# Performance work log

Measured on AMD Instinct MI355X. Metric: run time of the kernel, lower is better.

The kernel has to match this reference:

```python
import jax, jax.numpy as jnp
import numpy as np

BS, NPOINT, N, C = 2, 128, 8192, 128
NUM_CLASS, HEAD_BINS, K = 3, 12, 64
MLP1, MLP2, IOU_H = 128, 256, 128
EPS_BN = 1e-5


def setup_inputs():
    key = jax.random.key(0)
    ks = jax.random.split(key, 16)
    rn = lambda k, s, sc=1.0: jax.random.normal(k, s, jnp.float32) * sc
    return {
        'original_xyz': rn(ks[0], (BS, N, 3), 10.0),
        'original_feature': rn(ks[1], (BS, C, N)),
        'candidate_xyz': rn(ks[2], (BS, NPOINT, 3), 10.0),
        'pred_cls': rn(ks[3], (BS, NPOINT, NUM_CLASS)),
        'pred_offsets': rn(ks[4], (BS, NPOINT, 6)),
        'pred_angle_cls': rn(ks[5], (BS, NPOINT, HEAD_BINS)),
        'pred_angle_res': rn(ks[6], (BS, NPOINT, HEAD_BINS), 0.1),
        'w_mlp1': rn(ks[7], (MLP1, C + 3), 0.05), 'b_mlp1': jnp.zeros((MLP1,), jnp.float32),
        'w_mlp2': rn(ks[8], (MLP2, MLP1), 0.05), 'b_mlp2': jnp.zeros((MLP2,), jnp.float32),
        'w_iou0': rn(ks[9], (IOU_H, MLP2), 0.05), 'b_iou0': jnp.zeros((IOU_H,), jnp.float32),
        'g_iou0': jnp.ones((IOU_H,), jnp.float32), 'be_iou0': jnp.zeros((IOU_H,), jnp.float32),
        'w_iou1': rn(ks[10], (IOU_H, IOU_H), 0.05), 'b_iou1': jnp.zeros((IOU_H,), jnp.float32),
        'g_iou1': jnp.ones((IOU_H,), jnp.float32), 'be_iou1': jnp.zeros((IOU_H,), jnp.float32),
        'w_iou2': rn(ks[11], (1, IOU_H), 0.05), 'b_iou2': jnp.zeros((1,), jnp.float32),
    }


def _bn1d(x, g, b):
    # training-mode BatchNorm1d over (batch, length)
    m = jnp.mean(x, (0, 2), keepdims=True)
    v = jnp.var(x, (0, 2), keepdims=True)
    return (x - m) / jnp.sqrt(v + EPS_BN) * g[None, :, None] + b[None, :, None]


def _forward(original_xyz, original_feature, candidate_xyz, pred_cls, pred_offsets,
             pred_angle_cls, pred_angle_res, w_mlp1, b_mlp1, w_mlp2, b_mlp2,
             w_iou0, b_iou0, g_iou0, be_iou0, w_iou1, b_iou1, g_iou1, be_iou1,
             w_iou2, b_iou2):
    sg = jax.lax.stop_gradient
    original_xyz = sg(original_xyz)
    original_feature = sg(original_feature)
    bs, npoint = candidate_xyz.shape[0], candidate_xyz.shape[1]
    # --- decode_prediction (detached in original) ---
    acls = jnp.argmax(pred_angle_cls, -1)                              # [bs,np]
    ares = jnp.take_along_axis(pred_angle_res, acls[..., None], -1)[..., 0]
    apc = 2.0 * np.pi / HEAD_BINS
    angle = acls.astype(jnp.float32) * apc + ares
    heading = sg(jnp.where(angle > np.pi, angle - 2.0 * np.pi, angle))
    center = sg(candidate_xyz + pred_offsets[:, :, :3])
    lwh = sg(jnp.maximum(pred_offsets[:, :, 3:6] * 2.0, 0.1))
    # --- 4x4x4 grid scaled by box dims ---
    gs = jnp.linspace(-1.0, 1.0, 4)
    gx, gy, gz = jnp.meshgrid(gs, gs, gs, indexing='ij')
    grid = jnp.stack([gx.ravel(), gy.ravel(), gz.ravel()], -1)          # [64,3]
    whole_grid = grid[None, None] * lwh[:, :, None, :]                  # [bs,np,64,3]
    # --- rotation about z ---
    c, s = jnp.cos(heading), jnp.sin(heading)
    z = jnp.zeros_like(c); o = jnp.ones_like(c)
    R = jnp.stack([jnp.stack([c, s, z], -1),
                   jnp.stack([-s, c, z], -1),
                   jnp.stack([z, z, o], -1)], -2)                        # [bs,np,3,3]
    rel = jnp.einsum('bpkc,bpcd->bpkd', whole_grid, R)                   # [bs,np,64,3]
    corners = (rel + center[:, :, None, :]).reshape(bs, npoint * K, 3)   # [bs,M,3]
    # --- three_nn: 3 nearest original points per corner ---
    d2 = (jnp.sum(corners ** 2, -1)[:, :, None]
          + jnp.sum(original_xyz ** 2, -1)[:, None, :]
          - 2.0 * jnp.einsum('bmc,bnc->bmn', corners, original_xyz))     # [bs,M,N]
    _, idx = jax.lax.top_k(-d2, 3)                                       # [bs,M,3]
    nn_xyz = jax.vmap(lambda pts, i: pts[i])(original_xyz, idx)          # [bs,M,3,3]
    dist = jnp.sqrt(jnp.sum((nn_xyz - corners[:, :, None, :]) ** 2, -1)) # [bs,M,3]
    w = 1.0 / (dist + 1e-8)
    w = w / jnp.sum(w, -1, keepdims=True)
    nn_feat = jax.vmap(lambda f, i: f[:, i])(original_feature, idx)      # [bs,C,M,3]
    interp = jnp.sum(nn_feat * w[:, None], -1).reshape(bs, -1, npoint, K)
    feat = jnp.concatenate([rel.transpose(0, 3, 1, 2), interp], 1)       # [bs,C+3,np,K]
    # --- CGE shared MLP (1x1 conv + relu) ---
    h = jax.nn.relu(jnp.einsum('oc,bcpk->bopk', w_mlp1, feat) + b_mlp1[None, :, None, None])
    h = jax.nn.relu(jnp.einsum('oc,bcpk->bopk', w_mlp2, h) + b_mlp2[None, :, None, None])
    h = jnp.max(h, -1)                                                   # [bs,256,np]
    # --- IoU head ---
    h = jax.nn.relu(_bn1d(jnp.einsum('oc,bcp->bop', w_iou0, h) + b_iou0[None, :, None], g_iou0, be_iou0))
    h = jax.nn.relu(_bn1d(jnp.einsum('oc,bcp->bop', w_iou1, h) + b_iou1[None, :, None], g_iou1, be_iou1))
    return jnp.einsum('oc,bcp->bop', w_iou2, h) + b_iou2[None, :, None]  # [bs,1,np]


def reference(original_xyz, original_feature, candidate_xyz, pred_cls, pred_offsets,
              pred_angle_cls, pred_angle_res, w_mlp1, b_mlp1, w_mlp2, b_mlp2,
              w_iou0, b_iou0, g_iou0, be_iou0, w_iou1, b_iou1, g_iou1, be_iou1,
              w_iou2, b_iou2):
    return _forward(original_xyz, original_feature, candidate_xyz, pred_cls, pred_offsets,
                    pred_angle_cls, pred_angle_res, w_mlp1, b_mlp1, w_mlp2, b_mlp2,
                    w_iou0, b_iou0, g_iou0, be_iou0, w_iou1, b_iou1, g_iou1, be_iou1,
                    w_iou2, b_iou2)
```

## Files before the change

kernel.cpp:

```cpp
#include <hip/hip_runtime.h>
#include <math.h>

#define BSZ 2
#define NPOINT 128
#define NPTS 8192
#define CH_F 128
#define HEAD_BINS 12
#define KCOR 64
#define MTOT (NPOINT*KCOR)
#define FEAT_C 131
#define MLP2_C 256

#define OFF_CORNERS 0u
#define OFF_REL     196608u
#define OFF_IDX3    393216u
#define OFF_W3      589824u
#define OFF_FEATT   6684672u
#define OFF_W1T     15073280u
#define OFF_W2T     15140352u
#define OFF_XYZP    15271424u
#define OFF_H2      15533568u
#define OFF_X0      15795712u
#define OFF_X1      15926784u
#define OFF_BN0     16057856u
#define OFF_BN1     16058880u

__global__ __launch_bounds__(256) void k_prep(const float* __restrict__ cand, const float* __restrict__ offs,
                        const float* __restrict__ angc, const float* __restrict__ angr,
                        const float* __restrict__ w1, const float* __restrict__ w2,
                        const float* __restrict__ of, const float* __restrict__ xyz,
                        float* __restrict__ corners, float* __restrict__ rel,
                        float* __restrict__ w1t, float* __restrict__ w2t,
                        float* __restrict__ ft, float4* __restrict__ xyzp)
{
    __shared__ float tile[128][17];
    __shared__ float sr[4*KCOR*3];
    __shared__ float sc_[4*KCOR*3];
    int bid = blockIdx.x;
    int t = threadIdx.x;
    if (bid < 64) {
        int b = bid >> 5, p0 = (bid & 31) * 4;
        int lb = t >> 6, k = t & 63;
        int bp = b*NPOINT + p0 + lb;
        const float* ac = angc + bp*HEAD_BINS;
        int best = 0; float bv = ac[0];
        #pragma unroll
        for (int j = 1; j < HEAD_BINS; ++j) { float v = ac[j]; if (v > bv) { bv = v; best = j; } }
        float ares = angr[bp*HEAD_BINS + best];
        float angle = (float)best * 0.52359877559829882f + ares;
        float heading = (angle > 3.14159265358979323f) ? (angle - 6.28318530717958647f) : angle;
        float cx = cand[bp*3+0] + offs[bp*6+0];
        float cy = cand[bp*3+1] + offs[bp*6+1];
        float cz = cand[bp*3+2] + offs[bp*6+2];
        float dl = fmaxf(offs[bp*6+3]*2.0f, 0.1f);
        float dw = fmaxf(offs[bp*6+4]*2.0f, 0.1f);
        float dh = fmaxf(offs[bp*6+5]*2.0f, 0.1f);
        float chd = cosf(heading), shd = sinf(heading);
        int ix = (k>>4)&3, iy = (k>>2)&3, iz = k&3;
        float gx = (ix==3) ? 1.0f : (-1.0f + (2.0f/3.0f)*(float)ix);
        float gy = (iy==3) ? 1.0f : (-1.0f + (2.0f/3.0f)*(float)iy);
        float gz = (iz==3) ? 1.0f : (-1.0f + (2.0f/3.0f)*(float)iz);
        float wx = gx*dl, wy = gy*dw, wz = gz*dh;
        float rx = wx*chd - wy*shd;
        float ry = wx*shd + wy*chd;
        int si = (lb*KCOR + k)*3;
        sr[si+0] = rx;      sr[si+1] = ry;      sr[si+2] = wz;
        sc_[si+0] = rx+cx;  sc_[si+1] = ry+cy;  sc_[si+2] = wz+cz;
        __syncthreads();
        size_t base = ((size_t)b*MTOT + (size_t)p0*KCOR)*3;
        if (t < 192) {
            ((float4*)(rel + base))[t]     = ((const float4*)sr)[t];
            ((float4*)(corners + base))[t] = ((const float4*)sc_)[t];
        }
    } else if (bid < 80) {
        int i0 = (bid-64)*256 + t;
        for (int i = i0; i < FEAT_C*128; i += 16*256) { int o = i & 127, c = i >> 7; w1t[i] = w1[o*FEAT_C + c]; }
        for (int i = i0; i < 128*256;    i += 16*256) { int o = i & 255, c = i >> 8; w2t[i] = w2[o*128 + c]; }
    } else if (bid < 144) {
        int i = (bid-80)*256 + t;
        const float* s = xyz + (size_t)i*3;
        float x = s[0], y = s[1], z = s[2];
        xyzp[i] = make_float4(x, y, z, (x*x + y*y) + z*z);
    } else {
        int bi = bid - 144;
        int b = bi >> 9;
        int n0 = (bi & 511) * 16;
        #pragma unroll
        for (int it = 0; it < 2; ++it) {
            int id = it*256 + t;
            int c = id >> 2, q = id & 3;
            float4 v = *(const float4*)(of + ((size_t)(b*CH_F + c))*NPTS + n0 + q*4);
            tile[c][q*4+0] = v.x; tile[c][q*4+1] = v.y; tile[c][q*4+2] = v.z; tile[c][q*4+3] = v.w;
        }
        __syncthreads();
        #pragma unroll
        for (int it = 0; it < 2; ++it) {
            int id = it*256 + t;
            int n = id >> 5, cq = id & 31;
            float4 o;
            o.x = tile[cq*4+0][n]; o.y = tile[cq*4+1][n]; o.z = tile[cq*4+2][n]; o.w = tile[cq*4+3][n];
            *(float4*)(ft + ((size_t)b*NPTS + n0 + n)*CH_F + cq*4) = o;
        }
    }
}

__global__ __launch_bounds__(512) void k_three_nn(const float4* __restrict__ xyzp,
        const float* __restrict__ cand, const float* __restrict__ offs,
        const float* __restrict__ corners,
        int* __restrict__ idx3, float* __restrict__ w3)
{
    __shared__ unsigned short lidx[NPTS];
    __shared__ float4 ptile[512];
    __shared__ int    itile[512];
    __shared__ float  red[1752];
    __shared__ float  pms[512*3];
    __shared__ int    pmi[512*3];
    __shared__ int    s_cnt;
    __shared__ float  s_T;

    int bid = blockIdx.x;
    int b    = bid >> 8;
    int p    = (bid >> 1) & 127;
    int half = bid & 1;
    int t = threadIdx.x;
    int bp = b*NPOINT + p;

    float cx = cand[bp*3+0] + offs[bp*6+0];
    float cy = cand[bp*3+1] + offs[bp*6+1];
    float cz = cand[bp*3+2] + offs[bp*6+2];
    float dl = fmaxf(offs[bp*6+3]*2.0f, 0.1f);
    float dw = fmaxf(offs[bp*6+4]*2.0f, 0.1f);
    float dh = fmaxf(offs[bp*6+5]*2.0f, 0.1f);
    float H  = sqrtf((dl*dl + dw*dw) + dh*dh);
    float scc = (cx*cx + cy*cy) + cz*cz;

    const float4* xb = xyzp + (size_t)b*NPTS;

    float d2c[16];
    float a0 = 3.4e38f, a1 = 3.4e38f, a2 = 3.4e38f;
    #pragma unroll
    for (int i = 0; i < 16; ++i) {
        float4 P = xb[i*512 + t];
        float dot = fmaf(cz, P.z, fmaf(cy, P.y, cx*P.x));
        float d2 = (scc + P.w) - 2.0f*dot;
        d2c[i] = d2;
        a2 = __builtin_amdgcn_fmed3f(d2, a1, a2);
        a1 = __builtin_amdgcn_fmed3f(d2, a0, a1);
        a0 = fminf(d2, a0);
    }
    red[t*3+0] = a0; red[t*3+1] = a1; red[t*3+2] = a2;
    if (t == 0) s_cnt = 0;
    __syncthreads();
    if (t < 64) {
        float m0 = 3.4e38f, m1 = 3.4e38f, m2 = 3.4e38f;
        for (int s = t*8; s < t*8+8; ++s) {
            #pragma unroll
            for (int j = 0; j < 3; ++j) {
                float v = red[s*3+j];
                m2 = __builtin_amdgcn_fmed3f(v, m1, m2);
                m1 = __builtin_amdgcn_fmed3f(v, m0, m1);
                m0 = fminf(v, m0);
            }
        }
        red[1536 + t*3+0] = m0; red[1536 + t*3+1] = m1; red[1536 + t*3+2] = m2;
    }
    __syncthreads();
    if (t == 0) {
        float m0 = 3.4e38f, m1 = 3.4e38f, m2 = 3.4e38f;
        for (int s = 0; s < 64; ++s) {
            #pragma unroll
            for (int j = 0; j < 3; ++j) {
                float v = red[1536 + s*3+j];
                m2 = __builtin_amdgcn_fmed3f(v, m1, m2);
                m1 = __builtin_amdgcn_fmed3f(v, m0, m1);
                m0 = fminf(v, m0);
            }
        }
        float r3 = sqrtf(fmaxf(m2, 0.0f));
        float rad = r3 + 2.0f*H;
        s_T = rad*rad*1.0002f + 0.25f;
    }
    __syncthreads();

    float T = s_T;
    #pragma unroll
    for (int i = 0; i < 16; ++i) {
        if (d2c[i] <= T) {
            int pos = atomicAdd(&s_cnt, 1);
            lidx[pos] = (unsigned short)(i*512 + t);
        }
    }
    __syncthreads();
    int C = s_cnt;

    int ck  = half*32 + (t >> 4);
    int sub = t & 15;
    size_t crow = (size_t)b*MTOT + p*KCOR + ck;
    float ox = corners[crow*3+0], oy = corners[crow*3+1], oz = corners[crow*3+2];
    float so = (ox*ox + oy*oy) + oz*oz;
    float s0 = 3.4e38f, s1 = 3.4e38f, s2 = 3.4e38f;
    int i0 = 0x7fffffff, i1 = 0x7fffffff, i2 = 0x7fffffff;

    int ntile = (C + 511) >> 9;
    for (int tb = 0; tb < ntile; ++tb) {
        __syncthreads();
        int j = (tb << 9) + t;
        if (j < C) {
            int idx = lidx[j];
            ptile[t] = xb[idx];
            itile[t] = idx;
        } else {
            ptile[t] = make_float4(0.0f, 0.0f, 0.0f, 3.0e38f);
            itile[t] = 0x7fffffff;
        }
        __syncthreads();
        #pragma unroll 4
        for (int k = sub; k < 512; k += 16) {
            float4 P = ptile[k];
            int idx = itile[k];
            float dot = fmaf(oz, P.z, fmaf(oy, P.y, ox*P.x));
            float d2 = (so + P.w) - 2.0f*dot;
            bool lt0 = (d2 < s0) || (d2 == s0 && idx < i0);
            bool lt1 = (d2 < s1) || (d2 == s1 && idx < i1);
            bool lt2 = (d2 < s2) || (d2 == s2 && idx < i2);
            s2 = lt1 ? s1 : (lt2 ? d2  : s2); i2 = lt1 ? i1 : (lt2 ? idx : i2);
            s1 = lt0 ? s0 : (lt1 ? d2  : s1); i1 = lt0 ? i0 : (lt1 ? idx : i1);
            s0 = lt0 ? d2 : s0;               i0 = lt0 ? idx : i0;
        }
    }
    pms[t*3+0] = s0; pms[t*3+1] = s1; pms[t*3+2] = s2;
    pmi[t*3+0] = i0; pmi[t*3+1] = i1; pmi[t*3+2] = i2;
    __syncthreads();

    if (t < 32) {
        float f0 = 3.4e38f, f1 = 3.4e38f, f2 = 3.4e38f;
        int   j0 = 0x7fffffff, j1 = 0x7fffffff, j2 = 0x7fffffff;
        for (int tt = t*16; tt < t*16+16; ++tt) {
            #pragma unroll
            for (int j = 0; j < 3; ++j) {
                float d = pms[tt*3+j]; int id = pmi[tt*3+j];
                bool lt0 = (d < f0) || (d == f0 && id < j0);
                bool lt1 = (d < f1) || (d == f1 && id < j1);
                bool lt2 = (d < f2) || (d == f2 && id < j2);
                f2 = lt1 ? f1 : (lt2 ? d  : f2); j2 = lt1 ? j1 : (lt2 ? id : j2);
                f1 = lt0 ? f0 : (lt1 ? d  : f1); j1 = lt0 ? j0 : (lt1 ? id : j1);
                f0 = lt0 ? d  : f0;              j0 = lt0 ? id : j0;
            }
        }
        int ckf = half*32 + t;
        size_t row = (size_t)b*MTOT + p*KCOR + ckf;
        float qx = corners[row*3+0], qy = corners[row*3+1], qz = corners[row*3+2];
        int ii[3] = {j0, j1, j2};
        float w[3];
        #pragma unroll
        for (int j = 0; j < 3; ++j) {
            float4 P = xb[ii[j]];
            float dx = P.x - qx, dy = P.y - qy, dz = P.z - qz;
            float dist = sqrtf((dx*dx + dy*dy) + dz*dz);
            w[j] = 1.0f/(dist + 1e-8f);
        }
        float wsum = (w[0]+w[1])+w[2];
        #pragma unroll
        for (int j = 0; j < 3; ++j) {
            idx3[row*3+j] = ii[j];
            w3[row*3+j]   = w[j]/wsum;
        }
    }
}

__global__ __launch_bounds__(512) void k_mlp(const int* __restrict__ idx3, const float* __restrict__ w3,
        const float* __restrict__ featT, const float* __restrict__ rel,
        const float* __restrict__ w1t, const float* __restrict__ b1,
        const float* __restrict__ w2t, const float* __restrict__ b2,
        float* __restrict__ h2)
{
    __shared__ float lds[FEAT_C*64];
    __shared__ float swt[3][64];
    __shared__ int   sidx[3][64];
    int blk = blockIdx.x; int b = blk >> 7, p = blk & 127;
    int t = threadIdx.x;
    int g0 = b*MTOT + p*KCOR;

    if (t < 64) {
        size_t row = (size_t)(g0 + t)*3;
        #pragma unroll
        for (int j = 0; j < 3; ++j) { sidx[j][t] = idx3[row+j]; swt[j][t] = w3[row+j]; }
    } else if (t < 256) {
        int u = t - 64;
        lds[(u % 3)*64 + (u / 3)] = rel[(size_t)g0*3 + u];
    }
    __syncthreads();

    const float4* fb = (const float4*)(featT + (size_t)b*NPTS*CH_F);
    #pragma unroll
    for (int it = 0; it < 4; ++it) {
        int idx = it*512 + t;
        int cq = idx >> 6, m = idx & 63;
        int j0 = sidx[0][m], j1 = sidx[1][m], j2 = sidx[2][m];
        float w0 = swt[0][m], w1 = swt[1][m], w2 = swt[2][m];
        float4 f0 = fb[(size_t)j0*32 + cq];
        float4 f1 = fb[(size_t)j1*32 + cq];
        float4 f2 = fb[(size_t)j2*32 + cq];
        float4 v;
        v.x = (f0.x*w0 + f1.x*w1) + f2.x*w2;
        v.y = (f0.y*w0 + f1.y*w1) + f2.y*w2;
        v.z = (f0.z*w0 + f1.z*w1) + f2.z*w2;
        v.w = (f0.w*w0 + f1.w*w1) + f2.w*w2;
        int c0 = 3 + cq*4;
        lds[(c0+0)*64+m] = v.x; lds[(c0+1)*64+m] = v.y;
        lds[(c0+2)*64+m] = v.z; lds[(c0+3)*64+m] = v.w;
    }
    __syncthreads();

    int og = t >> 4, mg = t & 15;
    float acc[4][4];
    #pragma unroll
    for (int i = 0; i < 4; ++i) { float bb = b1[og*4+i];
        #pragma unroll
        for (int j = 0; j < 4; ++j) acc[i][j] = bb; }
    #pragma unroll 4
    for (int c = 0; c < FEAT_C; ++c) {
        float4 wv = *(const float4*)(w1t + c*128 + og*4);
        float4 f0 = *(const float4*)(&lds[c*64 + mg*4]);
        float fv[4] = {f0.x,f0.y,f0.z,f0.w};
        float wa[4] = {wv.x,wv.y,wv.z,wv.w};
        #pragma unroll
        for (int i = 0; i < 4; ++i)
            #pragma unroll
            for (int j = 0; j < 4; ++j)
                acc[i][j] = fmaf(wa[i], fv[j], acc[i][j]);
    }
    __syncthreads();
    #pragma unroll
    for (int i = 0; i < 4; ++i) {
        float4 r0 = make_float4(fmaxf(acc[i][0],0.f), fmaxf(acc[i][1],0.f), fmaxf(acc[i][2],0.f), fmaxf(acc[i][3],0.f));
        *(float4*)(&lds[(og*4+i)*64 + mg*4]) = r0;
    }
    __syncthreads();

    int og2 = t >> 3, mg2 = t & 7;
    float a2[4][8];
    #pragma unroll
    for (int i = 0; i < 4; ++i) { float bb = b2[og2*4+i];
        #pragma unroll
        for (int j = 0; j < 8; ++j) a2[i][j] = bb; }
    #pragma unroll 2
    for (int c = 0; c < 128; ++c) {
        float4 wv = *(const float4*)(w2t + c*MLP2_C + og2*4);
        float4 f0 = *(const float4*)(&lds[c*64 + mg2*8]);
        float4 f1 = *(const float4*)(&lds[c*64 + mg2*8 + 4]);
        float fv[8] = {f0.x,f0.y,f0.z,f0.w,f1.x,f1.y,f1.z,f1.w};
        float wa[4] = {wv.x,wv.y,wv.z,wv.w};
        #pragma unroll
        for (int i = 0; i < 4; ++i)
            #pragma unroll
            for (int j = 0; j < 8; ++j)
                a2[i][j] = fmaf(wa[i], fv[j], a2[i][j]);
    }
    float mx[4];
    #pragma unroll
    for (int i = 0; i < 4; ++i) {
        float m0 = a2[i][0];
        #pragma unroll
        for (int j = 1; j < 8; ++j) m0 = fmaxf(m0, a2[i][j]);
        mx[i] = fmaxf(m0, 0.0f);
    }
    #pragma unroll
    for (int off = 1; off < 8; off <<= 1)
        #pragma unroll
        for (int i = 0; i < 4; ++i)
            mx[i] = fmaxf(mx[i], __shfl_xor(mx[i], off, 64));
    if (mg2 == 0)
        *(float4*)(&h2[((size_t)b*NPOINT + p)*MLP2_C + og2*4]) = make_float4(mx[0],mx[1],mx[2],mx[3]);
}

__global__ __launch_bounds__(256) void k_head0(const float* __restrict__ h2, const float* __restrict__ w0,
                        const float* __restrict__ b0, const float* __restrict__ g0,
                        const float* __restrict__ be0,
                        float* __restrict__ x0, float* __restrict__ bn0)
{
    __shared__ float ssum[256], ssq[256];
    int o = blockIdx.x;
    int t = threadIdx.x;
    int b = t >> 7, p = t & 127;
    const float4* hb = (const float4*)(h2 + ((size_t)b*NPOINT + p)*MLP2_C);
    const float4* wr = (const float4*)(w0 + (size_t)o*MLP2_C);
    float acc = b0[o];
    #pragma unroll 8
    for (int cq = 0; cq < 64; ++cq) {
        float4 h = hb[cq], w = wr[cq];
        acc = fmaf(h.x, w.x, acc); acc = fmaf(h.y, w.y, acc);
        acc = fmaf(h.z, w.z, acc); acc = fmaf(h.w, w.w, acc);
    }
    x0[((size_t)b*NPOINT + p)*128 + o] = acc;
    ssum[t] = acc; ssq[t] = acc*acc;
    __syncthreads();
    if (t < 128) { ssum[t] += ssum[t+128]; ssq[t] += ssq[t+128]; }
    __syncthreads();
    if (t < 64) {
        float s = ssum[t] + ssum[t+64];
        float q = ssq[t] + ssq[t+64];
        #pragma unroll
        for (int off = 32; off >= 1; off >>= 1) {
            s += __shfl_down(s, off, 64);
            q += __shfl_down(q, off, 64);
        }
        if (t == 0) {
            float mean = s * (1.0f/256.0f);
            float var  = q * (1.0f/256.0f) - mean*mean;
            if (var < 0.f) var = 0.f;
            float scale = g0[o] / sqrtf(var + 1e-5f);
            bn0[o]       = scale;
            bn0[128 + o] = be0[o] - mean*scale;
        }
    }
}

__global__ __launch_bounds__(256) void k_head1(const float* __restrict__ x0, const float* __restrict__ bn0,
                        const float* __restrict__ w1, const float* __restrict__ b1,
                        const float* __restrict__ g1, const float* __restrict__ be1,
                        float* __restrict__ x1, float* __restrict__ bn1)
{
    __shared__ float ssum[256], ssq[256];
    int o = blockIdx.x;
    int t = threadIdx.x;
    int b = t >> 7, p = t & 127;
    const float4* xb = (const float4*)(x0 + ((size_t)b*NPOINT + p)*128);
    const float4* wr = (const float4*)(w1 + (size_t)o*128);
    float acc = b1[o];
    #pragma unroll 8
    for (int cq = 0; cq < 32; ++cq) {
        float4 xv = xb[cq], wv = wr[cq];
        float4 sc = *(const float4*)(bn0 + cq*4);
        float4 sh = *(const float4*)(bn0 + 128 + cq*4);
        acc = fmaf(wv.x, fmaxf(fmaf(xv.x, sc.x, sh.x), 0.0f), acc);
        acc = fmaf(wv.y, fmaxf(fmaf(xv.y, sc.y, sh.y), 0.0f), acc);
        acc = fmaf(wv.z, fmaxf(fmaf(xv.z, sc.z, sh.z), 0.0f), acc);
        acc = fmaf(wv.w, fmaxf(fmaf(xv.w, sc.w, sh.w), 0.0f), acc);
    }
    x1[((size_t)b*NPOINT + p)*128 + o] = acc;
    ssum[t] = acc; ssq[t] = acc*acc;
    __syncthreads();
    if (t < 128) { ssum[t] += ssum[t+128]; ssq[t] += ssq[t+128]; }
    __syncthreads();
    if (t < 64) {
        float s = ssum[t] + ssum[t+64];
        float q = ssq[t] + ssq[t+64];
        #pragma unroll
        for (int off = 32; off >= 1; off >>= 1) {
            s += __shfl_down(s, off, 64);
            q += __shfl_down(q, off, 64);
        }
        if (t == 0) {
            float mean = s * (1.0f/256.0f);
            float var  = q * (1.0f/256.0f) - mean*mean;
            if (var < 0.f) var = 0.f;
            float scale = g1[o] / sqrtf(var + 1e-5f);
            bn1[o]       = scale;
            bn1[128 + o] = be1[o] - mean*scale;
        }
    }
}

__global__ void k_final(const float* __restrict__ x1, const float* __restrict__ bn1,
                        const float* __restrict__ w2, const float* __restrict__ b2,
                        float* __restrict__ out)
{
    int t = threadIdx.x;
    int b = t >> 7, p = t & 127;
    const float4* xb = (const float4*)(x1 + ((size_t)b*NPOINT + p)*128);
    float acc = b2[0];
    #pragma unroll 8
    for (int cq = 0; cq < 32; ++cq) {
        float4 xv = xb[cq];
        float4 wv = *(const float4*)(w2 + cq*4);
        float4 sc = *(const float4*)(bn1 + cq*4);
        float4 sh = *(const float4*)(bn1 + 128 + cq*4);
        acc = fmaf(wv.x, fmaxf(fmaf(xv.x, sc.x, sh.x), 0.0f), acc);
        acc = fmaf(wv.y, fmaxf(fmaf(xv.y, sc.y, sh.y), 0.0f), acc);
        acc = fmaf(wv.z, fmaxf(fmaf(xv.z, sc.z, sh.z), 0.0f), acc);
        acc = fmaf(wv.w, fmaxf(fmaf(xv.w, sc.w, sh.w), 0.0f), acc);
    }
    out[b*NPOINT + p] = acc;
}

extern "C" void kernel_launch(void* const* d_in, const int* in_sizes, int n_in,
                              void* d_out, int out_size, void* d_ws, size_t ws_size,
                              hipStream_t stream)
{
    const float* xyz   = (const float*)d_in[0];
    const float* ofeat = (const float*)d_in[1];
    const float* cand  = (const float*)d_in[2];
    const float* offs  = (const float*)d_in[4];
    const float* angc  = (const float*)d_in[5];
    const float* angr  = (const float*)d_in[6];
    const float* w1    = (const float*)d_in[7];
    const float* b1    = (const float*)d_in[8];
    const float* w2    = (const float*)d_in[9];
    const float* b2    = (const float*)d_in[10];
    const float* wi0   = (const float*)d_in[11];
    const float* bi0   = (const float*)d_in[12];
    const float* gi0   = (const float*)d_in[13];
    const float* bei0  = (const float*)d_in[14];
    const float* wi1   = (const float*)d_in[15];
    const float* bi1   = (const float*)d_in[16];
    const float* gi1   = (const float*)d_in[17];
    const float* bei1  = (const float*)d_in[18];
    const float* wi2   = (const float*)d_in[19];
    const float* bi2   = (const float*)d_in[20];

    char* ws = (char*)d_ws;
    float*  corners = (float*)(ws + OFF_CORNERS);
    float*  rel     = (float*)(ws + OFF_REL);
    int*    idx3    = (int*)  (ws + OFF_IDX3);
    float*  w3      = (float*)(ws + OFF_W3);
    float*  featT   = (float*)(ws + OFF_FEATT);
    float*  w1t     = (float*)(ws + OFF_W1T);
    float*  w2t     = (float*)(ws + OFF_W2T);
    float4* xyzp    = (float4*)(ws + OFF_XYZP);
    float*  h2      = (float*)(ws + OFF_H2);
    float*  x0      = (float*)(ws + OFF_X0);
    float*  x1      = (float*)(ws + OFF_X1);
    float*  bn0     = (float*)(ws + OFF_BN0);
    float*  bn1     = (float*)(ws + OFF_BN1);

    k_prep     <<<1168, 256, 0, stream>>>(cand, offs, angc, angr, w1, w2, ofeat, xyz,
                                          corners, rel, w1t, w2t, featT, xyzp);
    k_three_nn <<<512, 512, 0, stream>>>(xyzp, cand, offs, corners, idx3, w3);
    k_mlp      <<<256, 512, 0, stream>>>(idx3, w3, featT, rel,
                                         w1t, b1, w2t, b2, h2);
    k_head0    <<<128, 256, 0, stream>>>(h2, wi0, bi0, gi0, bei0, x0, bn0);
    k_head1    <<<128, 256, 0, stream>>>(x0, bn0, wi1, bi1, gi1, bei1, x1, bn1);
    k_final    <<<1, 256, 0, stream>>>(x1, bn1, wi2, bi2, (float*)d_out);
}
```

Measured before the change: 218.7 us.

## Split three-NN into candidate-filter and chunked search kernels, merge partials in MLP

The old three-NN kernel did two jobs in one block: it built a per-proposal candidate list in LDS and then searched it, with 512 blocks. The candidate filtering now runs once per proposal in its own kernel and writes the list to global memory. The search is split across 4 chunks of up to 2048 candidates, giving 2048 blocks, and each chunk writes its partial top-3. The MLP kernel merges the partial top-3s and computes the interpolation weights. This raises parallelism when candidate lists are long, at the cost of an extra launch and more global traffic for the lists and partials.

Measured after the change: 229.9 us. 1.05x slower.

```diff
diff --git a/kernel.cpp b/kernel.cpp
--- a/kernel.cpp
+++ b/kernel.cpp
@@ -10,11 +10,14 @@
 #define MTOT (NPOINT*KCOR)
 #define FEAT_C 131
 #define MLP2_C 256
+#define NCHK 4
 
 #define OFF_CORNERS 0u
 #define OFF_REL     196608u
-#define OFF_IDX3    393216u
-#define OFF_W3      589824u
+#define OFF_PD      786432u
+#define OFF_PIX     1572864u
+#define OFF_CAND    2359296u
+#define OFF_CNT     6553600u
 #define OFF_FEATT   6684672u
 #define OFF_W1T     15073280u
 #define OFF_W2T     15140352u
@@ -104,24 +107,14 @@
     }
 }
 
-__global__ __launch_bounds__(512) void k_three_nn(const float4* __restrict__ xyzp,
+__global__ __launch_bounds__(512) void k_cand(const float4* __restrict__ xyzp,
         const float* __restrict__ cand, const float* __restrict__ offs,
-        const float* __restrict__ corners,
-        int* __restrict__ idx3, float* __restrict__ w3)
-{
-    __shared__ unsigned short lidx[NPTS];
-    __shared__ float4 ptile[512];
-    __shared__ int    itile[512];
-    __shared__ float  red[1752];
-    __shared__ float  pms[512*3];
-    __shared__ int    pmi[512*3];
-    __shared__ int    s_cnt;
-    __shared__ float  s_T;
-
-    int bid = blockIdx.x;
-    int b    = bid >> 8;
-    int p    = (bid >> 1) & 127;
-    int half = bid & 1;
+        unsigned short* __restrict__ candlist, int* __restrict__ cnt)
+{
+    __shared__ float red[1752];
+    __shared__ int   s_cnt;
+    int bx = blockIdx.x;
+    int b = bx >> 7, p = bx & 127;
     int t = threadIdx.x;
     int bp = b*NPOINT + p;
 
@@ -135,7 +128,6 @@
     float scc = (cx*cx + cy*cy) + cz*cz;
 
     const float4* xb = xyzp + (size_t)b*NPTS;
-
     float d2c[16];
     float a0 = 3.4e38f, a1 = 3.4e38f, a2 = 3.4e38f;
     #pragma unroll
@@ -165,6 +157,7 @@
         red[1536 + t*3+0] = m0; red[1536 + t*3+1] = m1; red[1536 + t*3+2] = m2;
     }
     __syncthreads();
+    __shared__ float s_T;
     if (t == 0) {
         float m0 = 3.4e38f, m1 = 3.4e38f, m2 = 3.4e38f;
         for (int s = 0; s < 64; ++s) {
@@ -181,32 +174,67 @@
         s_T = rad*rad*1.0002f + 0.25f;
     }
     __syncthreads();
-
     float T = s_T;
+    unsigned short* cl = candlist + (size_t)bx*NPTS;
     #pragma unroll
     for (int i = 0; i < 16; ++i) {
         if (d2c[i] <= T) {
             int pos = atomicAdd(&s_cnt, 1);
-            lidx[pos] = (unsigned short)(i*512 + t);
-        }
-    }
-    __syncthreads();
-    int C = s_cnt;
-
-    int ck  = half*32 + (t >> 4);
+            cl[pos] = (unsigned short)(i*512 + t);
+        }
+    }
+    __syncthreads();
+    if (t == 0) cnt[bx] = s_cnt;
+}
+
+__global__ __launch_bounds__(512) void k_three_nn(const float4* __restrict__ xyzp,
+        const float* __restrict__ corners,
+        const unsigned short* __restrict__ candlist, const int* __restrict__ cnt,
+        float* __restrict__ pd, int* __restrict__ pix)
+{
+    __shared__ float4 ptile[512];
+    __shared__ int    itile[512];
+    __shared__ float  pms[512*3];
+    __shared__ int    pmi[512*3];
+
+    int bid = blockIdx.x;
+    int chunk = bid & 3;
+    int hb = bid >> 2;
+    int b = hb >> 8, p = (hb >> 1) & 127, half = hb & 1;
+    int bx = b*NPOINT + p;
+    int t = threadIdx.x;
+    int C = cnt[bx];
+    int start = chunk << 11;
+    size_t cbase = (size_t)b*MTOT + p*KCOR + half*32;
+
+    if (start >= C) {
+        if (t < 96) {
+            int cc = t / 3, j = t - cc*3;
+            size_t row = cbase + cc;
+            pd [row*(NCHK*3) + chunk*3 + j] = 3.4e38f;
+            pix[row*(NCHK*3) + chunk*3 + j] = 0x7fffffff;
+        }
+        return;
+    }
+    int len = C - start; if (len > 2048) len = 2048;
+
+    const float4* xb = xyzp + (size_t)b*NPTS;
+    const unsigned short* cl = candlist + (size_t)bx*NPTS + start;
+
+    int cc  = t >> 4;
     int sub = t & 15;
-    size_t crow = (size_t)b*MTOT + p*KCOR + ck;
+    size_t crow = cbase + cc;
     float ox = corners[crow*3+0], oy = corners[crow*3+1], oz = corners[crow*3+2];
     float so = (ox*ox + oy*oy) + oz*oz;
     float s0 = 3.4e38f, s1 = 3.4e38f, s2 = 3.4e38f;
     int i0 = 0x7fffffff, i1 = 0x7fffffff, i2 = 0x7fffffff;
 
-    int ntile = (C + 511) >> 9;
+    int ntile = (len + 511) >> 9;
     for (int tb = 0; tb < ntile; ++tb) {
         __syncthreads();
         int j = (tb << 9) + t;
-        if (j < C) {
-            int idx = lidx[j];
+        if (j < len) {
+            int idx = cl[j];
             ptile[t] = xb[idx];
             itile[t] = idx;
         } else {
@@ -247,9 +275,43 @@
                 f0 = lt0 ? d  : f0;              j0 = lt0 ? id : j0;
             }
         }
-        int ckf = half*32 + t;
-        size_t row = (size_t)b*MTOT + p*KCOR + ckf;
+        size_t row = cbase + t;
+        float* pdr = pd  + row*(NCHK*3) + chunk*3;
+        int*   pir = pix + row*(NCHK*3) + chunk*3;
+        pdr[0] = f0; pdr[1] = f1; pdr[2] = f2;
+        pir[0] = j0; pir[1] = j1; pir[2] = j2;
+    }
+}
+
+__global__ __launch_bounds__(512) void k_mlp(const float4* __restrict__ xyzp, const float* __restrict__ corners,
+        const float* __restrict__ pd, const int* __restrict__ pix,
+        const float* __restrict__ featT, const float* __restrict__ rel,
+        const float* __restrict__ w1t, const float* __restrict__ b1,
+        const float* __restrict__ w2t, const float* __restrict__ b2,
+        float* __restrict__ h2)
+{
+    __shared__ float lds[FEAT_C*64];
+    __shared__ float swt[3][64];
+    __shared__ int   sidx[3][64];
+    int blk = blockIdx.x; int b = blk >> 7, p = blk & 127;
+    int t = threadIdx.x;
+    int g0 = b*MTOT + p*KCOR;
+
+    if (t < 64) {
+        size_t row = (size_t)(g0 + t);
+        float f0 = 3.4e38f, f1 = 3.4e38f, f2 = 3.4e38f;
+        int   j0 = 0x7fffffff, j1 = 0x7fffffff, j2 = 0x7fffffff;
+        for (int k = 0; k < NCHK*3; ++k) {
+            float d = pd[row*(NCHK*3) + k]; int id = pix[row*(NCHK*3) + k];
+            bool lt0 = (d < f0) || (d == f0 && id < j0);
+            bool lt1 = (d < f1) || (d == f1 && id < j1);
+            bool lt2 = (d < f2) || (d == f2 && id < j2);
+            f2 = lt1 ? f1 : (lt2 ? d  : f2); j2 = lt1 ? j1 : (lt2 ? id : j2);
+            f1 = lt0 ? f0 : (lt1 ? d  : f1); j1 = lt0 ? j0 : (lt1 ? id : j1);
+            f0 = lt0 ? d  : f0;              j0 = lt0 ? id : j0;
+        }
         float qx = corners[row*3+0], qy = corners[row*3+1], qz = corners[row*3+2];
+        const float4* xb = xyzp + (size_t)b*NPTS;
         int ii[3] = {j0, j1, j2};
         float w[3];
         #pragma unroll
@@ -261,30 +323,7 @@
         }
         float wsum = (w[0]+w[1])+w[2];
         #pragma unroll
-        for (int j = 0; j < 3; ++j) {
-            idx3[row*3+j] = ii[j];
-            w3[row*3+j]   = w[j]/wsum;
-        }
-    }
-}
-
-__global__ __launch_bounds__(512) void k_mlp(const int* __restrict__ idx3, const float* __restrict__ w3,
-        const float* __restrict__ featT, const float* __restrict__ rel,
-        const float* __restrict__ w1t, const float* __restrict__ b1,
-        const float* __restrict__ w2t, const float* __restrict__ b2,
-        float* __restrict__ h2)
-{
-    __shared__ float lds[FEAT_C*64];
-    __shared__ float swt[3][64];
-    __shared__ int   sidx[3][64];
-    int blk = blockIdx.x; int b = blk >> 7, p = blk & 127;
-    int t = threadIdx.x;
-    int g0 = b*MTOT + p*KCOR;
-
-    if (t < 64) {
-        size_t row = (size_t)(g0 + t)*3;
-        #pragma unroll
-        for (int j = 0; j < 3; ++j) { sidx[j][t] = idx3[row+j]; swt[j][t] = w3[row+j]; }
+        for (int j = 0; j < 3; ++j) { sidx[j][t] = ii[j]; swt[j][t] = w[j]/wsum; }
     } else if (t < 256) {
         int u = t - 64;
         lds[(u % 3)*64 + (u / 3)] = rel[(size_t)g0*3 + u];
@@ -512,8 +551,10 @@
     char* ws = (char*)d_ws;
     float*  corners = (float*)(ws + OFF_CORNERS);
     float*  rel     = (float*)(ws + OFF_REL);
-    int*    idx3    = (int*)  (ws + OFF_IDX3);
-    float*  w3      = (float*)(ws + OFF_W3);
+    float*  pd      = (float*)(ws + OFF_PD);
+    int*    pix     = (int*)  (ws + OFF_PIX);
+    unsigned short* candlist = (unsigned short*)(ws + OFF_CAND);
+    int*    cnt     = (int*)  (ws + OFF_CNT);
     float*  featT   = (float*)(ws + OFF_FEATT);
     float*  w1t     = (float*)(ws + OFF_W1T);
     float*  w2t     = (float*)(ws + OFF_W2T);
@@ -526,8 +567,9 @@
 
     k_prep     <<<1168, 256, 0, stream>>>(cand, offs, angc, angr, w1, w2, ofeat, xyz,
                                           corners, rel, w1t, w2t, featT, xyzp);
-    k_three_nn <<<512, 512, 0, stream>>>(xyzp, cand, offs, corners, idx3, w3);
-    k_mlp      <<<256, 512, 0, stream>>>(idx3, w3, featT, rel,
+    k_cand     <<<256, 512, 0, stream>>>(xyzp, cand, offs, candlist, cnt);
+    k_three_nn <<<2048, 512, 0, stream>>>(xyzp, corners, candlist, cnt, pd, pix);
+    k_mlp      <<<256, 512, 0, stream>>>(xyzp, corners, pd, pix, featT, rel,
                                          w1t, b1, w2t, b2, h2);
     k_head0    <<<128, 256, 0, stream>>>(h2, wi0, bi0, gi0, bei0, x0, bn0);
     k_head1    <<<128, 256, 0, stream>>>(x0, bn0, wi1, bi1, gi1, bei1, x1, bn1);
```
